# Optimization experiments

Hardware: AMD Instinct MI355X
Metric: run time of the kernel (lower is better)

Reference implementation:

```python
import jax, jax.numpy as jnp
import numpy as np

N, H, W, C, CK, ITER = 4, 256, 256, 8, 2, 4
HID = 2 * C
C2 = C * C


def project(x, w1, b1, w2, b2, w3, b3):
    # flax Project: Dense->gelu->Dense->gelu->Dense (gelu approximate=tanh, jax default)
    h = jax.nn.gelu(x @ w1 + b1)
    h = jax.nn.gelu(h @ w2 + b2)
    return h @ w3 + b3


def setup_inputs() -> dict:
    key = jax.random.key(0)
    ks = jax.random.split(key, 40)
    d = {}
    d['u'] = jax.random.normal(ks[0], (N, H, W, C), jnp.float32)
    d['k'] = jax.random.normal(ks[1], (N, H, W, CK), jnp.float32)
    idx = 2
    # gamma MLP (in CK), delta MLP (in CK), greens real/imag MLPs (in 2)
    for nm, fin in zip(['g', 'dl', 'fr', 'fi'], [CK, CK, 2, 2]):
        for li, (fi_, fo) in enumerate([(fin, HID), (HID, HID), (HID, C2)]):
            d[f'{nm}_w{li+1}'] = jax.random.normal(ks[idx], (fi_, fo), jnp.float32) / np.sqrt(fi_).astype(np.float32)
            d[f'{nm}_b{li+1}'] = jnp.zeros((fo,), jnp.float32)
            idx += 1
    d['bias'] = jax.random.normal(ks[idx], (C,), jnp.float32)
    return d


def reference(u, k, g_w1, g_b1, g_w2, g_b2, g_w3, g_b3,
              dl_w1, dl_b1, dl_w2, dl_b2, dl_w3, dl_b3,
              fr_w1, fr_b1, fr_w2, fr_b2, fr_w3, fr_b3,
              fi_w1, fi_b1, fi_w2, fi_b2, fi_w3, fi_b3, bias):
    # per-pixel gamma / delta matrices: (N,H,W,C,C), scaled by 1/C^2 as in original
    gmat = (project(k, g_w1, g_b1, g_w2, g_b2, g_w3, g_b3) / C2).reshape(N, H, W, C, C)
    dmat = (project(k, dl_w1, dl_b1, dl_w2, dl_b2, dl_w3, dl_b3) / C2).reshape(N, H, W, C, C)
    # spectral Green's filter on the rfft grid; meshgrid(kx, ky) -> (W, H//2+1)
    kx = jnp.fft.rfftfreq(H, d=1.0 / H)
    ky = jnp.fft.fftfreq(W, d=1.0 / W)
    Kx, Ky = jnp.meshgrid(kx, ky)
    K = jnp.stack([Kx, Ky], axis=-1).astype(jnp.float32)  # (W, H//2+1, 2)
    filt_r = project(K, fr_w1, fr_b1, fr_w2, fr_b2, fr_w3, fr_b3)
    filt_i = project(K, fi_w1, fi_b1, fi_w2, fi_b2, fi_w3, fi_b3)
    filt = ((filt_r + 1j * filt_i) / C2).reshape(W, H // 2 + 1, C, C)  # H==W
    for _ in range(ITER):
        local = 2.0 * u - jnp.einsum('nhwj,nhwjk->nhwk', u, gmat)
        du = jnp.einsum('nhwj,nhwjk->nhwk', u, dmat)
        uf = jnp.fft.rfftn(du, axes=(1, 2))  # (N,H,W//2+1,C) complex
        gu = jnp.fft.irfftn(jnp.einsum('nhwj,hwjk->nhwk', uf, filt), axes=(1, 2))
        u = local + jnp.einsum('nhwj,nhwjk->nhwk', gu, gmat)
    return jax.nn.gelu(u + bias)
```

## Files before the change

kernel.cpp:

```cpp
#include <hip/hip_runtime.h>
#include <math.h>

#define NB 4
#define HB 256
#define WB 256
#define CB 8
#define NPIX (NB*HB*WB)
#define W2B 129
#define TWO_PI_F 6.283185307179586f

typedef float f32x4 __attribute__((ext_vector_type(4)));

__device__ __forceinline__ float gelu_f(float x){
    float z = 0.7978845608028654f*(x + 0.044715f*x*x*x);
    return x * __builtin_amdgcn_rcpf(1.0f + __expf(-2.0f*z));
}

__device__ __forceinline__ unsigned pack_bf16x2(float a, float b){
    unsigned ua = __float_as_uint(a), ub = __float_as_uint(b);
    ua = (ua + 0x7FFFu + ((ua >> 16) & 1u)) >> 16;
    ub = (ub + 0x7FFFu + ((ub >> 16) & 1u)) >> 16;
    return ua | (ub << 16);
}
__device__ __forceinline__ float2 unpack_bf16x2(unsigned v){
    return make_float2(__uint_as_float(v << 16), __uint_as_float(v & 0xFFFF0000u));
}

__device__ __forceinline__ void ldcp(float* dst, const float* __restrict__ src, int n, int t){
    for (int i = t; i < n; i += 256) dst[i] = src[i];
}

__global__ __launch_bounds__(256) void prep_kernel(
    const float* __restrict__ kin,
    const float* gw1,const float* gb1,const float* gw2,const float* gb2,const float* gw3,const float* gb3,
    const float* dw1,const float* db1,const float* dw2,const float* db2,const float* dw3,const float* db3,
    const float* fw1,const float* fb1,const float* fw2,const float* fb2,const float* fw3,const float* fb3,
    const float* iw1,const float* ib1,const float* iw2,const float* ib2,const float* iw3,const float* ib3,
    unsigned* __restrict__ gmat, unsigned* __restrict__ dmat,
    unsigned* __restrict__ fpack)
{
    __shared__ __align__(16) float sw[2816];
    int t = threadIdx.x;
    int b = blockIdx.x;
    if (b >= 129){
        int gd = (b >= 1153);
        const float* w1 = gd ? dw1 : gw1;  const float* b1 = gd ? db1 : gb1;
        const float* w2 = gd ? dw2 : gw2;  const float* b2 = gd ? db2 : gb2;
        const float* w3 = gd ? dw3 : gw3;  const float* b3 = gd ? db3 : gb3;
        ldcp(sw+0,   w1,  32, t); ldcp(sw+32,  b1, 16, t);
        ldcp(sw+48,  w2, 256, t); ldcp(sw+304, b2, 16, t);
        ldcp(sw+320, w3,1024, t); ldcp(sw+1344,b3, 64, t);
        __syncthreads();
        unsigned* mat = gd ? dmat : gmat;
        int pix = (b - (gd ? 1153 : 129))*256 + t;
        float2 kv = ((const float2*)kin)[pix];
        size_t base = (size_t)(pix >> 6)*2048 + (pix & 63);
        float h1[16], h2[16];
#pragma unroll
        for (int o = 0; o < 16; ++o)
            h1[o] = gelu_f(kv.x*sw[o] + kv.y*sw[16+o] + sw[32+o]);
#pragma unroll
        for (int oc = 0; oc < 4; ++oc){
            f32x4 acc = *(const f32x4*)(sw + 304 + oc*4);
#pragma unroll
            for (int i = 0; i < 16; ++i){
                f32x4 w = *(const f32x4*)(sw + 48 + i*16 + oc*4);
                acc += h1[i]*w;
            }
            h2[oc*4+0] = gelu_f(acc.x); h2[oc*4+1] = gelu_f(acc.y);
            h2[oc*4+2] = gelu_f(acc.z); h2[oc*4+3] = gelu_f(acc.w);
        }
        const float s = 1.0f/64.0f;
#pragma unroll
        for (int oc = 0; oc < 16; ++oc){
            f32x4 acc = *(const f32x4*)(sw + 1344 + oc*4);
#pragma unroll
            for (int i = 0; i < 16; ++i){
                f32x4 w = *(const f32x4*)(sw + 320 + i*64 + oc*4);
                acc += h2[i]*w;
            }
            mat[base + (size_t)(oc*2+0)*64] = pack_bf16x2(acc.x*s, acc.y*s);
            mat[base + (size_t)(oc*2+1)*64] = pack_bf16x2(acc.z*s, acc.w*s);
        }
    } else {
        ldcp(sw+0,   fw1,  32, t); ldcp(sw+32,  fb1, 16, t);
        ldcp(sw+48,  fw2, 256, t); ldcp(sw+304, fb2, 16, t);
        ldcp(sw+320, fw3,1024, t); ldcp(sw+1344,fb3, 64, t);
        ldcp(sw+1408+0,   iw1,  32, t); ldcp(sw+1408+32,  ib1, 16, t);
        ldcp(sw+1408+48,  iw2, 256, t); ldcp(sw+1408+304, ib2, 16, t);
        ldcp(sw+1408+320, iw3,1024, t); ldcp(sw+1408+1344,ib3, 64, t);
        __syncthreads();
        int w2 = b;
        float x = (float)w2;
        float y = (float)(t < 128 ? t : t - 256);
        float h1r[16], h1i[16], h2r[16], h2i[16];
#pragma unroll
        for (int o = 0; o < 16; ++o){
            h1r[o] = gelu_f(x*sw[o] + y*sw[16+o] + sw[32+o]);
            h1i[o] = gelu_f(x*sw[1408+o] + y*sw[1408+16+o] + sw[1408+32+o]);
        }
#pragma unroll
        for (int o = 0; o < 16; ++o){
            float ar = sw[304+o], ai = sw[1408+304+o];
#pragma unroll
            for (int i = 0; i < 16; ++i){
                ar += h1r[i]*sw[48+i*16+o];
                ai += h1i[i]*sw[1408+48+i*16+o];
            }
            h2r[o] = gelu_f(ar); h2i[o] = gelu_f(ai);
        }
        unsigned* dst = fpack + (size_t)w2*16384 + t;
        const float s = 1.0f/64.0f;
#pragma unroll
        for (int o = 0; o < 64; ++o){
            float ar = sw[1344+o], ai = sw[1408+1344+o];
#pragma unroll
            for (int i = 0; i < 16; ++i){
                ar += h2r[i]*sw[320+i*64+o];
                ai += h2i[i]*sw[1408+320+i*64+o];
            }
            dst[o*256] = pack_bf16x2(ar*s, ai*s);
        }
    }
}

__device__ __forceinline__ void fft256v(f32x4* xr, f32x4* xi, int t, float sgn)
{
    int n2 = t >> 4, k1 = t & 15;
    float csA, snA; __sincosf(sgn*TWO_PI_F*(float)k1*(1.0f/16.0f), &snA, &csA);
    f32x4 ar = {0.f,0.f,0.f,0.f}, ai = {0.f,0.f,0.f,0.f};
    float cw = 1.f, sw = 0.f;
#pragma unroll
    for (int n1 = 0; n1 < 16; ++n1){
        f32x4 vr = xr[16*n1 + n2], vi = xi[16*n1 + n2];
        ar += vr*cw - vi*sw;
        ai += vr*sw + vi*cw;
        float cn = cw*csA - sw*snA;
        sw = cw*snA + sw*csA; cw = cn;
    }
    float cs2, sn2; __sincosf(sgn*TWO_PI_F*(float)(n2*k1)*(1.0f/256.0f), &sn2, &cs2);
    f32x4 br = ar*cs2 - ai*sn2;
    f32x4 bi = ar*sn2 + ai*cs2;
    __syncthreads();
    xr[t] = br; xi[t] = bi;
    __syncthreads();
    int k1b = t & 15, k2 = t >> 4;
    float csB, snB; __sincosf(sgn*TWO_PI_F*(float)k2*(1.0f/16.0f), &snB, &csB);
    f32x4 yr = {0.f,0.f,0.f,0.f}, yi = {0.f,0.f,0.f,0.f};
    cw = 1.f; sw = 0.f;
#pragma unroll
    for (int n2b = 0; n2b < 16; ++n2b){
        f32x4 br2 = xr[n2b*16 + k1b], bi2 = xi[n2b*16 + k1b];
        yr += br2*cw - bi2*sw;
        yi += br2*sw + bi2*cw;
        float cn = cw*csB - sw*snB;
        sw = cw*snB + sw*csB; cw = cn;
    }
    __syncthreads();
    xr[t] = yr; xi[t] = yi;
    __syncthreads();
}

__device__ __forceinline__ void fft256v_core(f32x4* xr, f32x4* xi, int t, float sgn,
                                             f32x4& outR, f32x4& outI)
{
    int n2 = t >> 4, k1 = t & 15;
    float csA, snA; __sincosf(sgn*TWO_PI_F*(float)k1*(1.0f/16.0f), &snA, &csA);
    f32x4 ar = {0.f,0.f,0.f,0.f}, ai = {0.f,0.f,0.f,0.f};
    float cw = 1.f, sw = 0.f;
#pragma unroll
    for (int n1 = 0; n1 < 16; ++n1){
        f32x4 vr = xr[16*n1 + n2], vi = xi[16*n1 + n2];
        ar += vr*cw - vi*sw;
        ai += vr*sw + vi*cw;
        float cn = cw*csA - sw*snA;
        sw = cw*snA + sw*csA; cw = cn;
    }
    float cs2, sn2; __sincosf(sgn*TWO_PI_F*(float)(n2*k1)*(1.0f/256.0f), &sn2, &cs2);
    f32x4 br = ar*cs2 - ai*sn2;
    f32x4 bi = ar*sn2 + ai*cs2;
    __syncthreads();
    xr[t] = br; xi[t] = bi;
    __syncthreads();
    int k1b = t & 15, k2 = t >> 4;
    float csB, snB; __sincosf(sgn*TWO_PI_F*(float)k2*(1.0f/16.0f), &snB, &csB);
    f32x4 yr = {0.f,0.f,0.f,0.f}, yi = {0.f,0.f,0.f,0.f};
    cw = 1.f; sw = 0.f;
#pragma unroll
    for (int n2b = 0; n2b < 16; ++n2b){
        f32x4 br2 = xr[n2b*16 + k1b], bi2 = xi[n2b*16 + k1b];
        yr += br2*cw - bi2*sw;
        yi += br2*sw + bi2*cw;
        float cn = cw*csB - sw*snB;
        sw = cw*snB + sw*csB; cw = cn;
    }
    outR = yr; outI = yi;
}

__device__ __forceinline__ void fwd_store(
    f32x4* XR, f32x4* XI, const float* dv, int t, int n, int h,
    float2* __restrict__ spec)
{
    XR[t] = (f32x4){dv[0],dv[2],dv[4],dv[6]};
    XI[t] = (f32x4){dv[1],dv[3],dv[5],dv[7]};
    __syncthreads();
    fft256v(XR, XI, t, -1.f);
    if (t <= 128){
        int m = (256 - t) & 255;
        f32x4 zr = XR[t], zi = XI[t], yr = XR[m], yi = XI[m];
        float4* dst = (float4*)(spec + (((size_t)n*129 + t)*256 + h)*8);
        dst[0] = make_float4(0.5f*(zr.x+yr.x), 0.5f*(zi.x-yi.x), 0.5f*(zi.x+yi.x), 0.5f*(yr.x-zr.x));
        dst[1] = make_float4(0.5f*(zr.y+yr.y), 0.5f*(zi.y-yi.y), 0.5f*(zi.y+yi.y), 0.5f*(yr.y-zr.y));
        dst[2] = make_float4(0.5f*(zr.z+yr.z), 0.5f*(zi.z-yi.z), 0.5f*(zi.z+yi.z), 0.5f*(yr.z-zr.z));
        dst[3] = make_float4(0.5f*(zr.w+yr.w), 0.5f*(zi.w-yi.w), 0.5f*(zi.w+yi.w), 0.5f*(yr.w-zr.w));
    }
}

__device__ __forceinline__ void inv_fft_to_gu(
    const float2* __restrict__ spec, f32x4* XR, f32x4* XI,
    int t, int n, int h, float* gu)
{
    int w2 = (t <= 128) ? t : 256 - t;
    const float4* rp = (const float4*)(spec + (((size_t)n*129 + w2)*256 + h)*8);
    float4 q0 = rp[0], q1 = rp[1], q2 = rp[2], q3 = rp[3];
    f32x4 xr, xi;
    if (t <= 128){
        xr = (f32x4){q0.x - q0.w, q1.x - q1.w, q2.x - q2.w, q3.x - q3.w};
        xi = (f32x4){q0.y + q0.z, q1.y + q1.z, q2.y + q2.z, q3.y + q3.z};
    } else {
        xr = (f32x4){ q0.x + q0.w,  q1.x + q1.w,  q2.x + q2.w,  q3.x + q3.w};
        xi = (f32x4){-q0.y + q0.z, -q1.y + q1.z, -q2.y + q2.z, -q3.y + q3.z};
    }
    XR[t] = xr; XI[t] = xi;
    __syncthreads();
    f32x4 gr, gi;
    fft256v_core(XR, XI, t, +1.f, gr, gi);
    const float s = 1.0f/65536.0f;
    gu[0]=gr.x*s; gu[1]=gi.x*s; gu[2]=gr.y*s; gu[3]=gi.y*s;
    gu[4]=gr.z*s; gu[5]=gi.z*s; gu[6]=gr.w*s; gu[7]=gi.w*s;
}

__global__ __launch_bounds__(256) void fft_fwd_kernel(
    const float* __restrict__ u, const unsigned* __restrict__ dmat,
    float2* __restrict__ spec)
{
    __shared__ f32x4 XR[256], XI[256];
    int t = threadIdx.x, bid = blockIdx.x;
    int n = bid >> 8, h = bid & 255;
    const float* up = u + (size_t)bid*2048 + (size_t)t*8;
    float4 ua = ((const float4*)up)[0], ub = ((const float4*)up)[1];
    float uv[8] = {ua.x,ua.y,ua.z,ua.w, ub.x,ub.y,ub.z,ub.w};
    const unsigned* dp = dmat + ((size_t)bid*4 + (t>>6))*2048 + (t&63);
    float dv[8];
#pragma unroll
    for (int k = 0; k < 8; ++k) dv[k] = 0.f;
#pragma unroll
    for (int j = 0; j < 8; ++j){
        float uj = uv[j];
#pragma unroll
        for (int k2 = 0; k2 < 4; ++k2){
            float2 f = unpack_bf16x2(dp[(j*4+k2)*64]);
            dv[2*k2]   += uj * f.x;
            dv[2*k2+1] += uj * f.y;
        }
    }
    fwd_store(XR, XI, dv, t, n, h, spec);
}

__global__ __launch_bounds__(512) void ffth_mult_kernel(
    float2* __restrict__ spec, const unsigned* __restrict__ fpack)
{
    __shared__ f32x4 XR[2][256], XI[2][256];
    int tid = threadIdx.x;
    int t = tid & 255, g = tid >> 8;
    int c0 = g*4;
    int n = blockIdx.x / 129, w2 = blockIdx.x % 129;
    float2* base = spec + ((size_t)(n*129 + w2))*2048;
    const float4* rp = (const float4*)(base + (size_t)t*8);
    float4 ra = rp[g*2], rb = rp[g*2+1];
    XR[g][t] = (f32x4){ra.x, ra.z, rb.x, rb.z};
    XI[g][t] = (f32x4){ra.y, ra.w, rb.y, rb.w};
    __syncthreads();
    f32x4 sR, sI;
    fft256v_core(XR[g], XI[g], t, -1.f, sR, sI);
    __syncthreads();
    XR[g][t] = sR; XI[g][t] = sI;
    __syncthreads();
    f32x4 oR = XR[1-g][t], oI = XI[1-g][t];
    f32x4 aR = g ? oR : sR, aI = g ? oI : sI;
    f32x4 bR = g ? sR : oR, bI = g ? sI : oI;
    float sr[8] = {aR.x,aR.y,aR.z,aR.w, bR.x,bR.y,bR.z,bR.w};
    float si[8] = {aI.x,aI.y,aI.z,aI.w, bI.x,bI.y,bI.z,bI.w};
    f32x4 orr = {0.f,0.f,0.f,0.f}, oii = {0.f,0.f,0.f,0.f};
    const unsigned* fp = fpack + (size_t)w2*16384 + t;
#pragma unroll
    for (int j = 0; j < 8; ++j){
        float sjr = sr[j], sji = si[j];
        float2 f0 = unpack_bf16x2(fp[(j*8 + c0 + 0)*256]);
        float2 f1 = unpack_bf16x2(fp[(j*8 + c0 + 1)*256]);
        float2 f2 = unpack_bf16x2(fp[(j*8 + c0 + 2)*256]);
        float2 f3 = unpack_bf16x2(fp[(j*8 + c0 + 3)*256]);
        orr.x += sjr*f0.x - sji*f0.y;  oii.x += sjr*f0.y + sji*f0.x;
        orr.y += sjr*f1.x - sji*f1.y;  oii.y += sjr*f1.y + sji*f1.x;
        orr.z += sjr*f2.x - sji*f2.y;  oii.z += sjr*f2.y + sji*f2.x;
        orr.w += sjr*f3.x - sji*f3.y;  oii.w += sjr*f3.y + sji*f3.x;
    }
    __syncthreads();
    XR[g][t] = orr; XI[g][t] = oii;
    __syncthreads();
    f32x4 vR, vI;
    fft256v_core(XR[g], XI[g], t, +1.f, vR, vI);
    float4* wp = (float4*)(base + (size_t)t*8);
    wp[g*2]   = make_float4(vR.x, vI.x, vR.y, vI.y);
    wp[g*2+1] = make_float4(vR.z, vI.z, vR.w, vI.w);
}

__global__ __launch_bounds__(256) void born_step_kernel(
    float2* __restrict__ spec, const float* __restrict__ u_in,
    float* __restrict__ u_out, const unsigned* __restrict__ gmat,
    const unsigned* __restrict__ dmat)
{
    __shared__ f32x4 XR[256], XI[256];
    int t = threadIdx.x, bid = blockIdx.x;
    int n = bid >> 8, h = bid & 255;
    float gu[8];
    inv_fft_to_gu(spec, XR, XI, t, n, h, gu);

    const float* up = u_in + (size_t)bid*2048 + (size_t)t*8;
    float4 ua = ((const float4*)up)[0], ub = ((const float4*)up)[1];
    float uv[8] = {ua.x,ua.y,ua.z,ua.w, ub.x,ub.y,ub.z,ub.w};
    float e[8], acc[8];
#pragma unroll
    for (int c = 0; c < 8; ++c){ e[c] = gu[c] - uv[c]; acc[c] = 2.0f*uv[c]; }
    const unsigned* gp = gmat + ((size_t)bid*4 + (t>>6))*2048 + (t&63);
#pragma unroll
    for (int j = 0; j < 8; ++j){
        float ej = e[j];
#pragma unroll
        for (int k2 = 0; k2 < 4; ++k2){
            float2 f = unpack_bf16x2(gp[(j*4+k2)*64]);
            acc[2*k2]   += ej * f.x;
            acc[2*k2+1] += ej * f.y;
        }
    }
    float* op = u_out + (size_t)bid*2048 + (size_t)t*8;
    ((float4*)op)[0] = make_float4(acc[0],acc[1],acc[2],acc[3]);
    ((float4*)op)[1] = make_float4(acc[4],acc[5],acc[6],acc[7]);

    const unsigned* dp = dmat + ((size_t)bid*4 + (t>>6))*2048 + (t&63);
    float dv[8];
#pragma unroll
    for (int k = 0; k < 8; ++k) dv[k] = 0.f;
#pragma unroll
    for (int j = 0; j < 8; ++j){
        float uj = acc[j];
#pragma unroll
        for (int k2 = 0; k2 < 4; ++k2){
            float2 f = unpack_bf16x2(dp[(j*4+k2)*64]);
            dv[2*k2]   += uj * f.x;
            dv[2*k2+1] += uj * f.y;
        }
    }
    __syncthreads();
    fwd_store(XR, XI, dv, t, n, h, spec);
}

__global__ __launch_bounds__(256) void final_kernel(
    const float2* __restrict__ spec, const float* __restrict__ u_in,
    const unsigned* __restrict__ gmat, const float* __restrict__ bias,
    float* __restrict__ out)
{
    __shared__ f32x4 XR[256], XI[256];
    int t = threadIdx.x, bid = blockIdx.x;
    int n = bid >> 8, h = bid & 255;
    float gu[8];
    inv_fft_to_gu(spec, XR, XI, t, n, h, gu);

    const float* up = u_in + (size_t)bid*2048 + (size_t)t*8;
    float4 ua = ((const float4*)up)[0], ub = ((const float4*)up)[1];
    float uv[8] = {ua.x,ua.y,ua.z,ua.w, ub.x,ub.y,ub.z,ub.w};
    float e[8], acc[8];
#pragma unroll
    for (int c = 0; c < 8; ++c){ e[c] = gu[c] - uv[c]; acc[c] = 2.0f*uv[c]; }
    const unsigned* gp = gmat + ((size_t)bid*4 + (t>>6))*2048 + (t&63);
#pragma unroll
    for (int j = 0; j < 8; ++j){
        float ej = e[j];
#pragma unroll
        for (int k2 = 0; k2 < 4; ++k2){
            float2 f = unpack_bf16x2(gp[(j*4+k2)*64]);
            acc[2*k2]   += ej * f.x;
            acc[2*k2+1] += ej * f.y;
        }
    }
#pragma unroll
    for (int k = 0; k < 8; ++k) acc[k] = gelu_f(acc[k] + bias[k]);
    float* op = out + (size_t)bid*2048 + (size_t)t*8;
    ((float4*)op)[0] = make_float4(acc[0],acc[1],acc[2],acc[3]);
    ((float4*)op)[1] = make_float4(acc[4],acc[5],acc[6],acc[7]);
}

extern "C" void kernel_launch(void* const* d_in, const int* in_sizes, int n_in,
                              void* d_out, int out_size, void* d_ws, size_t ws_size,
                              hipStream_t stream) {
    const float* u_in = (const float*)d_in[0];
    const float* k_in = (const float*)d_in[1];
    const float* Wp[24];
    for (int i = 0; i < 24; ++i) Wp[i] = (const float*)d_in[2+i];
    const float* bias = (const float*)d_in[26];

    char* base = (char*)d_ws;
    unsigned* gmat  = (unsigned*)(base);
    unsigned* dmat  = (unsigned*)(base + 33554432ull);
    unsigned* fpack = (unsigned*)(base + 67108864ull);
    float*    u_ws  = (float*)   (base + 75563008ull);
    float2*   spec  = (float2*)  (base + 83951616ull);

    prep_kernel<<<2177, 256, 0, stream>>>(k_in,
        Wp[0],Wp[1],Wp[2],Wp[3],Wp[4],Wp[5],
        Wp[6],Wp[7],Wp[8],Wp[9],Wp[10],Wp[11],
        Wp[12],Wp[13],Wp[14],Wp[15],Wp[16],Wp[17],
        Wp[18],Wp[19],Wp[20],Wp[21],Wp[22],Wp[23],
        gmat, dmat, fpack);

    fft_fwd_kernel<<<1024, 256, 0, stream>>>(u_in, dmat, spec);
    for (int it = 0; it < 4; ++it){
        ffth_mult_kernel<<<516, 512, 0, stream>>>(spec, fpack);
        if (it < 3){
            born_step_kernel<<<1024, 256, 0, stream>>>(
                spec, (it == 0) ? u_in : u_ws, u_ws, gmat, dmat);
        } else {
            final_kernel<<<1024, 256, 0, stream>>>(spec, u_ws, gmat, bias, (float*)d_out);
        }
    }
}
```

Baseline: 220.7 us.

## Repack gamma/delta/filter matrices for 128-bit loads and process two pixels per thread

The bf16 per-pixel matrices and the spectral filter are reordered so that each thread's four consecutive packed words sit together. Every consumer can then fetch them with one uint4 load instead of four strided 32-bit loads. The prep kernel now computes two pixels per thread, halving the grid and reusing the shared-memory weight reads across both pixels. The trade-off is higher register pressure in prep, and the layout change must stay consistent across all consumer kernels.

Measured after the change: 220.1 us. Within noise of the previous version (-0.3%).

```diff
diff --git a/kernel.cpp b/kernel.cpp
--- a/kernel.cpp
+++ b/kernel.cpp
@@ -43,7 +43,7 @@
     int t = threadIdx.x;
     int b = blockIdx.x;
     if (b >= 129){
-        int gd = (b >= 1153);
+        int gd = (b >= 641);
         const float* w1 = gd ? dw1 : gw1;  const float* b1 = gd ? db1 : gb1;
         const float* w2 = gd ? dw2 : gw2;  const float* b2 = gd ? db2 : gb2;
         const float* w3 = gd ? dw3 : gw3;  const float* b3 = gd ? db3 : gb3;
@@ -52,35 +52,53 @@
         ldcp(sw+320, w3,1024, t); ldcp(sw+1344,b3, 64, t);
         __syncthreads();
         unsigned* mat = gd ? dmat : gmat;
-        int pix = (b - (gd ? 1153 : 129))*256 + t;
-        float2 kv = ((const float2*)kin)[pix];
-        size_t base = (size_t)(pix >> 6)*2048 + (pix & 63);
-        float h1[16], h2[16];
-#pragma unroll
-        for (int o = 0; o < 16; ++o)
-            h1[o] = gelu_f(kv.x*sw[o] + kv.y*sw[16+o] + sw[32+o]);
+        int p0 = (b - (gd ? 641 : 129))*512 + t;
+        int p1 = p0 + 256;
+        float2 kv0 = ((const float2*)kin)[p0];
+        float2 kv1 = ((const float2*)kin)[p1];
+        size_t base0 = (size_t)(p0 >> 6)*2048 + (size_t)(p0 & 63)*4;
+        size_t base1 = (size_t)(p1 >> 6)*2048 + (size_t)(p1 & 63)*4;
+        float h1[2][16], h2[2][16];
+#pragma unroll
+        for (int o = 0; o < 16; ++o){
+            float wx = sw[o], wy = sw[16+o], bo = sw[32+o];
+            h1[0][o] = gelu_f(kv0.x*wx + kv0.y*wy + bo);
+            h1[1][o] = gelu_f(kv1.x*wx + kv1.y*wy + bo);
+        }
 #pragma unroll
         for (int oc = 0; oc < 4; ++oc){
-            f32x4 acc = *(const f32x4*)(sw + 304 + oc*4);
+            f32x4 bb = *(const f32x4*)(sw + 304 + oc*4);
+            f32x4 a0 = bb, a1 = bb;
 #pragma unroll
             for (int i = 0; i < 16; ++i){
                 f32x4 w = *(const f32x4*)(sw + 48 + i*16 + oc*4);
-                acc += h1[i]*w;
+                a0 += h1[0][i]*w; a1 += h1[1][i]*w;
             }
-            h2[oc*4+0] = gelu_f(acc.x); h2[oc*4+1] = gelu_f(acc.y);
-            h2[oc*4+2] = gelu_f(acc.z); h2[oc*4+3] = gelu_f(acc.w);
+            h2[0][oc*4+0]=gelu_f(a0.x); h2[0][oc*4+1]=gelu_f(a0.y);
+            h2[0][oc*4+2]=gelu_f(a0.z); h2[0][oc*4+3]=gelu_f(a0.w);
+            h2[1][oc*4+0]=gelu_f(a1.x); h2[1][oc*4+1]=gelu_f(a1.y);
+            h2[1][oc*4+2]=gelu_f(a1.z); h2[1][oc*4+3]=gelu_f(a1.w);
         }
         const float s = 1.0f/64.0f;
 #pragma unroll
-        for (int oc = 0; oc < 16; ++oc){
-            f32x4 acc = *(const f32x4*)(sw + 1344 + oc*4);
+        for (int j = 0; j < 8; ++j){
+            f32x4 bA = *(const f32x4*)(sw + 1344 + j*8);
+            f32x4 bB = *(const f32x4*)(sw + 1344 + j*8 + 4);
+            f32x4 A0 = bA, A1 = bB, B0 = bA, B1 = bB;
 #pragma unroll
             for (int i = 0; i < 16; ++i){
-                f32x4 w = *(const f32x4*)(sw + 320 + i*64 + oc*4);
-                acc += h2[i]*w;
+                f32x4 wA = *(const f32x4*)(sw + 320 + i*64 + j*8);
+                f32x4 wB = *(const f32x4*)(sw + 320 + i*64 + j*8 + 4);
+                float h0 = h2[0][i], h1v = h2[1][i];
+                A0 += h0*wA; A1 += h0*wB;
+                B0 += h1v*wA; B1 += h1v*wB;
             }
-            mat[base + (size_t)(oc*2+0)*64] = pack_bf16x2(acc.x*s, acc.y*s);
-            mat[base + (size_t)(oc*2+1)*64] = pack_bf16x2(acc.z*s, acc.w*s);
+            uint4 o0 = { pack_bf16x2(A0.x*s,A0.y*s), pack_bf16x2(A0.z*s,A0.w*s),
+                         pack_bf16x2(A1.x*s,A1.y*s), pack_bf16x2(A1.z*s,A1.w*s) };
+            uint4 o1 = { pack_bf16x2(B0.x*s,B0.y*s), pack_bf16x2(B0.z*s,B0.w*s),
+                         pack_bf16x2(B1.x*s,B1.y*s), pack_bf16x2(B1.z*s,B1.w*s) };
+            *(uint4*)(mat + base0 + (size_t)j*256) = o0;
+            *(uint4*)(mat + base1 + (size_t)j*256) = o1;
         }
     } else {
         ldcp(sw+0,   fw1,  32, t); ldcp(sw+32,  fb1, 16, t);
@@ -109,17 +127,19 @@
             }
             h2r[o] = gelu_f(ar); h2i[o] = gelu_f(ai);
         }
-        unsigned* dst = fpack + (size_t)w2*16384 + t;
         const float s = 1.0f/64.0f;
 #pragma unroll
-        for (int o = 0; o < 64; ++o){
-            float ar = sw[1344+o], ai = sw[1408+1344+o];
+        for (int q = 0; q < 16; ++q){
+            f32x4 aR = *(const f32x4*)(sw + 1344 + q*4);
+            f32x4 aI = *(const f32x4*)(sw + 1408 + 1344 + q*4);
 #pragma unroll
             for (int i = 0; i < 16; ++i){
-                ar += h2r[i]*sw[320+i*64+o];
-                ai += h2i[i]*sw[1408+320+i*64+o];
+                aR += h2r[i] * *(const f32x4*)(sw + 320 + i*64 + q*4);
+                aI += h2i[i] * *(const f32x4*)(sw + 1408 + 320 + i*64 + q*4);
             }
-            dst[o*256] = pack_bf16x2(ar*s, ai*s);
+            uint4 out = { pack_bf16x2(aR.x*s, aI.x*s), pack_bf16x2(aR.y*s, aI.y*s),
+                          pack_bf16x2(aR.z*s, aI.z*s), pack_bf16x2(aR.w*s, aI.w*s) };
+            *(uint4*)(fpack + (size_t)w2*16384 + (size_t)q*1024 + (size_t)t*4) = out;
         }
     }
 }
@@ -240,6 +260,23 @@
     gu[4]=gr.z*s; gu[5]=gi.z*s; gu[6]=gr.w*s; gu[7]=gi.w*s;
 }
 
+__device__ __forceinline__ void matvec_acc(const unsigned* __restrict__ mat,
+                                           size_t base, const float* v, float* acc)
+{
+    const uint4* mp = (const uint4*)(mat + base);
+#pragma unroll
+    for (int j = 0; j < 8; ++j){
+        uint4 q = mp[j*64];
+        float vj = v[j];
+        float2 f0 = unpack_bf16x2(q.x), f1 = unpack_bf16x2(q.y);
+        float2 f2 = unpack_bf16x2(q.z), f3 = unpack_bf16x2(q.w);
+        acc[0] += vj*f0.x; acc[1] += vj*f0.y;
+        acc[2] += vj*f1.x; acc[3] += vj*f1.y;
+        acc[4] += vj*f2.x; acc[5] += vj*f2.y;
+        acc[6] += vj*f3.x; acc[7] += vj*f3.y;
+    }
+}
+
 __global__ __launch_bounds__(256) void fft_fwd_kernel(
     const float* __restrict__ u, const unsigned* __restrict__ dmat,
     float2* __restrict__ spec)
@@ -250,20 +287,9 @@
     const float* up = u + (size_t)bid*2048 + (size_t)t*8;
     float4 ua = ((const float4*)up)[0], ub = ((const float4*)up)[1];
     float uv[8] = {ua.x,ua.y,ua.z,ua.w, ub.x,ub.y,ub.z,ub.w};
-    const unsigned* dp = dmat + ((size_t)bid*4 + (t>>6))*2048 + (t&63);
-    float dv[8];
-#pragma unroll
-    for (int k = 0; k < 8; ++k) dv[k] = 0.f;
-#pragma unroll
-    for (int j = 0; j < 8; ++j){
-        float uj = uv[j];
-#pragma unroll
-        for (int k2 = 0; k2 < 4; ++k2){
-            float2 f = unpack_bf16x2(dp[(j*4+k2)*64]);
-            dv[2*k2]   += uj * f.x;
-            dv[2*k2+1] += uj * f.y;
-        }
-    }
+    size_t base = (size_t)(bid*4 + (t>>6))*2048 + (size_t)(t&63)*4;
+    float dv[8] = {0,0,0,0,0,0,0,0};
+    matvec_acc(dmat, base, uv, dv);
     fwd_store(XR, XI, dv, t, n, h, spec);
 }
 
@@ -273,7 +299,6 @@
     __shared__ f32x4 XR[2][256], XI[2][256];
     int tid = threadIdx.x;
     int t = tid & 255, g = tid >> 8;
-    int c0 = g*4;
     int n = blockIdx.x / 129, w2 = blockIdx.x % 129;
     float2* base = spec + ((size_t)(n*129 + w2))*2048;
     const float4* rp = (const float4*)(base + (size_t)t*8);
@@ -292,14 +317,13 @@
     float sr[8] = {aR.x,aR.y,aR.z,aR.w, bR.x,bR.y,bR.z,bR.w};
     float si[8] = {aI.x,aI.y,aI.z,aI.w, bI.x,bI.y,bI.z,bI.w};
     f32x4 orr = {0.f,0.f,0.f,0.f}, oii = {0.f,0.f,0.f,0.f};
-    const unsigned* fp = fpack + (size_t)w2*16384 + t;
+    const uint4* fp = (const uint4*)(fpack + (size_t)w2*16384 + (size_t)t*4);
 #pragma unroll
     for (int j = 0; j < 8; ++j){
         float sjr = sr[j], sji = si[j];
-        float2 f0 = unpack_bf16x2(fp[(j*8 + c0 + 0)*256]);
-        float2 f1 = unpack_bf16x2(fp[(j*8 + c0 + 1)*256]);
-        float2 f2 = unpack_bf16x2(fp[(j*8 + c0 + 2)*256]);
-        float2 f3 = unpack_bf16x2(fp[(j*8 + c0 + 3)*256]);
+        uint4 fq = fp[(j*2 + g)*256];
+        float2 f0 = unpack_bf16x2(fq.x), f1 = unpack_bf16x2(fq.y);
+        float2 f2 = unpack_bf16x2(fq.z), f3 = unpack_bf16x2(fq.w);
         orr.x += sjr*f0.x - sji*f0.y;  oii.x += sjr*f0.y + sji*f0.x;
         orr.y += sjr*f1.x - sji*f1.y;  oii.y += sjr*f1.y + sji*f1.x;
         orr.z += sjr*f2.x - sji*f2.y;  oii.z += sjr*f2.y + sji*f2.x;
@@ -332,35 +356,14 @@
     float e[8], acc[8];
 #pragma unroll
     for (int c = 0; c < 8; ++c){ e[c] = gu[c] - uv[c]; acc[c] = 2.0f*uv[c]; }
-    const unsigned* gp = gmat + ((size_t)bid*4 + (t>>6))*2048 + (t&63);
-#pragma unroll
-    for (int j = 0; j < 8; ++j){
-        float ej = e[j];
-#pragma unroll
-        for (int k2 = 0; k2 < 4; ++k2){
-            float2 f = unpack_bf16x2(gp[(j*4+k2)*64]);
-            acc[2*k2]   += ej * f.x;
-            acc[2*k2+1] += ej * f.y;
-        }
-    }
+    size_t base = (size_t)(bid*4 + (t>>6))*2048 + (size_t)(t&63)*4;
+    matvec_acc(gmat, base, e, acc);
     float* op = u_out + (size_t)bid*2048 + (size_t)t*8;
     ((float4*)op)[0] = make_float4(acc[0],acc[1],acc[2],acc[3]);
     ((float4*)op)[1] = make_float4(acc[4],acc[5],acc[6],acc[7]);
 
-    const unsigned* dp = dmat + ((size_t)bid*4 + (t>>6))*2048 + (t&63);
-    float dv[8];
-#pragma unroll
-    for (int k = 0; k < 8; ++k) dv[k] = 0.f;
-#pragma unroll
-    for (int j = 0; j < 8; ++j){
-        float uj = acc[j];
-#pragma unroll
-        for (int k2 = 0; k2 < 4; ++k2){
-            float2 f = unpack_bf16x2(dp[(j*4+k2)*64]);
-            dv[2*k2]   += uj * f.x;
-            dv[2*k2+1] += uj * f.y;
-        }
-    }
+    float dv[8] = {0,0,0,0,0,0,0,0};
+    matvec_acc(dmat, base, acc, dv);
     __syncthreads();
     fwd_store(XR, XI, dv, t, n, h, spec);
 }
@@ -382,17 +385,8 @@
     float e[8], acc[8];
 #pragma unroll
     for (int c = 0; c < 8; ++c){ e[c] = gu[c] - uv[c]; acc[c] = 2.0f*uv[c]; }
-    const unsigned* gp = gmat + ((size_t)bid*4 + (t>>6))*2048 + (t&63);
-#pragma unroll
-    for (int j = 0; j < 8; ++j){
-        float ej = e[j];
-#pragma unroll
-        for (int k2 = 0; k2 < 4; ++k2){
-            float2 f = unpack_bf16x2(gp[(j*4+k2)*64]);
-            acc[2*k2]   += ej * f.x;
-            acc[2*k2+1] += ej * f.y;
-        }
-    }
+    size_t base = (size_t)(bid*4 + (t>>6))*2048 + (size_t)(t&63)*4;
+    matvec_acc(gmat, base, e, acc);
 #pragma unroll
     for (int k = 0; k < 8; ++k) acc[k] = gelu_f(acc[k] + bias[k]);
     float* op = out + (size_t)bid*2048 + (size_t)t*8;
@@ -416,7 +410,7 @@
     float*    u_ws  = (float*)   (base + 75563008ull);
     float2*   spec  = (float2*)  (base + 83951616ull);
 
-    prep_kernel<<<2177, 256, 0, stream>>>(k_in,
+    prep_kernel<<<1153, 256, 0, stream>>>(k_in,
         Wp[0],Wp[1],Wp[2],Wp[3],Wp[4],Wp[5],
         Wp[6],Wp[7],Wp[8],Wp[9],Wp[10],Wp[11],
         Wp[12],Wp[13],Wp[14],Wp[15],Wp[16],Wp[17],
```
